# Optimization experiments

Measured on AMD Instinct MI355X. Metric: run time of the kernel, lower is better.

Reference implementation:

```python
import jax, jax.numpy as jnp
import numpy as np

A = 5.0  # smoothness parameter


def setup_inputs() -> dict:
    key = jax.random.key(0)
    kx, kw = jax.random.split(key)
    x = jax.random.uniform(kx, (4096, 256), dtype=jnp.float32)
    weight = jax.random.uniform(kw, (256, 256), dtype=jnp.float32)
    return {"x": x, "weight": weight}


def reference(x, weight):
    # inner: [batch, in_features, out_features] broadcast elementwise max
    inner = jnp.maximum(x[..., None], weight[None])
    # smooth min over in_features (dim=-2): -(1/a) * logsumexp(-a * inner)
    smooth = -jax.nn.logsumexp(-A * inner, axis=-2) / A
    # hard min over same dim
    hard = jnp.min(inner, axis=-2)
    # straight-through estimator: forward value = hard, gradient flows via smooth
    return jax.lax.stop_gradient(hard - smooth) + smooth
```

## Files before the change

kernel.cpp:

```cpp
#include <hip/hip_runtime.h>


typedef _Float16 h2 __attribute__((ext_vector_type(2)));
typedef int i16v __attribute__((ext_vector_type(16)));

__global__ __launch_bounds__(256)
void prepack_kernel(const float* __restrict__ x, const float* __restrict__ w,
                    unsigned int* __restrict__ xt, unsigned int* __restrict__ wq) {
    const int tid = blockIdx.x * 256 + threadIdx.x;
    if (tid < 524288) {
        const int j  = tid & 3;
        const int rr = (tid >> 2) & 3;
        const int c  = (tid >> 4) & 31;
        const int r4 = tid >> 9;
        const int row = (r4 << 2) + rr;
        const float2 v = *reinterpret_cast<const float2*>(&x[(size_t)row * 256 + (c << 3) + (j << 1)]);
        const h2 p = h2{(_Float16)v.x, (_Float16)v.y};
        xt[tid] = __builtin_bit_cast(unsigned int, p);
    } else {
        const int u   = tid - 524288;
        const int col = u & 255;
        const int j   = (u >> 8) & 3;
        const int c   = u >> 10;
        const int i0  = (c << 3) + (j << 1);
        const h2 p = h2{(_Float16)w[(size_t)i0 * 256 + col], (_Float16)w[(size_t)(i0 + 1) * 256 + col]};
        const int idx = ((((c >> 1) << 8) + col) << 3) + ((c & 1) << 2) + j;
        wq[(size_t)idx] = __builtin_bit_cast(unsigned int, p);
    }
}

#define PKSTEP(XS, WV, ACC) do { int _t;                                     \
    asm("v_pk_max_f16 %0, %2, %3\n\t"                                        \
        "v_pk_min_f16 %1, %1, %0"                                            \
        : "=&v"(_t), "+v"(ACC) : "s"(XS), "v"(WV)); } while (0)

#define STEPC(Xv, Wv) do {                                                   \
    PKSTEP(Xv[0],  Wv.x, acc0); PKSTEP(Xv[4],  Wv.x, acc1);                  \
    PKSTEP(Xv[8],  Wv.x, acc2); PKSTEP(Xv[12], Wv.x, acc3);                  \
    PKSTEP(Xv[1],  Wv.y, acc0); PKSTEP(Xv[5],  Wv.y, acc1);                  \
    PKSTEP(Xv[9],  Wv.y, acc2); PKSTEP(Xv[13], Wv.y, acc3);                  \
    PKSTEP(Xv[2],  Wv.z, acc0); PKSTEP(Xv[6],  Wv.z, acc1);                  \
    PKSTEP(Xv[10], Wv.z, acc2); PKSTEP(Xv[14], Wv.z, acc3);                  \
    PKSTEP(Xv[3],  Wv.w, acc0); PKSTEP(Xv[7],  Wv.w, acc1);                  \
    PKSTEP(Xv[11], Wv.w, acc2); PKSTEP(Xv[15], Wv.w, acc3); } while (0)

#define WAITALL() do {                                                       \
    asm volatile("s_waitcnt lgkmcnt(0) vmcnt(0)" ::: "memory");              \
    __builtin_amdgcn_sched_barrier(0); } while (0)

#define PF_SC(XA_, XB_, WA_, WB_, SC) do {                                   \
    const unsigned long long _xs = xa + (unsigned long long)(((SC) & 15) << 7); \
    const unsigned int _wo = wo + (unsigned int)(((SC) & 15) << 13);         \
    asm volatile("s_load_dwordx16 %0, %2, 0x0\n\t"                           \
                 "s_load_dwordx16 %1, %2, 0x40"                              \
                 : "=&s"(XA_), "=&s"(XB_) : "s"(_xs));                       \
    asm volatile("global_load_dwordx4 %0, %2, %3\n\t"                        \
                 "global_load_dwordx4 %1, %2, %3 offset:16"                  \
                 : "=&v"(WA_), "=&v"(WB_) : "v"(_wo), "s"(wb)); } while (0)

#define STAGE(K, CXA, CXB, CWA, CWB, NXA, NXB, NWA, NWB)                     \
    WAITALL();                                                               \
    if ((K) < 15) PF_SC(NXA, NXB, NWA, NWB, s0 + (K) + 1);                   \
    STEPC(CXA, CWA); STEPC(CXB, CWB);

__global__ __launch_bounds__(256, 4)
void stemm_main(const unsigned int* __restrict__ xt, const unsigned int* __restrict__ wq,
                float* __restrict__ out) {
    const int t    = threadIdx.x;
    const int lane = t & 63;
    const int wv   = __builtin_amdgcn_readfirstlane(t >> 6);
    const int c0   = (blockIdx.x & 3) << 6;
    const int rb   = blockIdx.x >> 2;
    const int r4   = (rb << 2) + wv;
    const int s0   = wv << 2;

    const unsigned long long xa = (unsigned long long)xt + ((unsigned long long)r4 << 11);
    const unsigned int       wo = (unsigned int)((c0 + lane) << 5);
    const unsigned long long wb = (unsigned long long)wq;

    i16v X0a{}, X0b{}, X1a{}, X1b{};
    uint4 W0a{0,0,0,0}, W0b{0,0,0,0}, W1a{0,0,0,0}, W1b{0,0,0,0};

    h2 acc0 = h2{(_Float16)65504.0f, (_Float16)65504.0f};
    h2 acc1 = acc0, acc2 = acc0, acc3 = acc0;

    PF_SC(X0a, X0b, W0a, W0b, s0);

    STAGE(0,  X0a, X0b, W0a, W0b,  X1a, X1b, W1a, W1b)
    STAGE(1,  X1a, X1b, W1a, W1b,  X0a, X0b, W0a, W0b)
    STAGE(2,  X0a, X0b, W0a, W0b,  X1a, X1b, W1a, W1b)
    STAGE(3,  X1a, X1b, W1a, W1b,  X0a, X0b, W0a, W0b)
    STAGE(4,  X0a, X0b, W0a, W0b,  X1a, X1b, W1a, W1b)
    STAGE(5,  X1a, X1b, W1a, W1b,  X0a, X0b, W0a, W0b)
    STAGE(6,  X0a, X0b, W0a, W0b,  X1a, X1b, W1a, W1b)
    STAGE(7,  X1a, X1b, W1a, W1b,  X0a, X0b, W0a, W0b)
    STAGE(8,  X0a, X0b, W0a, W0b,  X1a, X1b, W1a, W1b)
    STAGE(9,  X1a, X1b, W1a, W1b,  X0a, X0b, W0a, W0b)
    STAGE(10, X0a, X0b, W0a, W0b,  X1a, X1b, W1a, W1b)
    STAGE(11, X1a, X1b, W1a, W1b,  X0a, X0b, W0a, W0b)
    STAGE(12, X0a, X0b, W0a, W0b,  X1a, X1b, W1a, W1b)
    STAGE(13, X1a, X1b, W1a, W1b,  X0a, X0b, W0a, W0b)
    STAGE(14, X0a, X0b, W0a, W0b,  X1a, X1b, W1a, W1b)
    STAGE(15, X1a, X1b, W1a, W1b,  X0a, X0b, W0a, W0b)

    const int r0 = r4 << 2;
    out[(size_t)(r0 + 0) * 256 + c0 + lane] = fminf((float)acc0.x, (float)acc0.y);
    out[(size_t)(r0 + 1) * 256 + c0 + lane] = fminf((float)acc1.x, (float)acc1.y);
    out[(size_t)(r0 + 2) * 256 + c0 + lane] = fminf((float)acc2.x, (float)acc2.y);
    out[(size_t)(r0 + 3) * 256 + c0 + lane] = fminf((float)acc3.x, (float)acc3.y);
}

extern "C" void kernel_launch(void* const* d_in, const int* in_sizes, int n_in,
                              void* d_out, int out_size, void* d_ws, size_t ws_size,
                              hipStream_t stream) {
    const float* x = (const float*)d_in[0];
    const float* w = (const float*)d_in[1];
    float* out = (float*)d_out;

    unsigned int* xt = (unsigned int*)d_ws;
    unsigned int* wq = (unsigned int*)((char*)d_ws + (2u << 20));

    hipLaunchKernelGGL(prepack_kernel, dim3(2176), dim3(256), 0, stream, x, w, xt, wq);
    hipLaunchKernelGGL(stemm_main, dim3(1024), dim3(256), 0, stream, xt, wq, out);
}
```

Before: 21.40 us.

## Fuse fp16 prepack into main kernel, staging weights in LDS

```diff
diff --git a/kernel.cpp b/kernel.cpp
--- a/kernel.cpp
+++ b/kernel.cpp
@@ -4,29 +4,8 @@
 typedef _Float16 h2 __attribute__((ext_vector_type(2)));
 typedef int i16v __attribute__((ext_vector_type(16)));
 
-__global__ __launch_bounds__(256)
-void prepack_kernel(const float* __restrict__ x, const float* __restrict__ w,
-                    unsigned int* __restrict__ xt, unsigned int* __restrict__ wq) {
-    const int tid = blockIdx.x * 256 + threadIdx.x;
-    if (tid < 524288) {
-        const int j  = tid & 3;
-        const int rr = (tid >> 2) & 3;
-        const int c  = (tid >> 4) & 31;
-        const int r4 = tid >> 9;
-        const int row = (r4 << 2) + rr;
-        const float2 v = *reinterpret_cast<const float2*>(&x[(size_t)row * 256 + (c << 3) + (j << 1)]);
-        const h2 p = h2{(_Float16)v.x, (_Float16)v.y};
-        xt[tid] = __builtin_bit_cast(unsigned int, p);
-    } else {
-        const int u   = tid - 524288;
-        const int col = u & 255;
-        const int j   = (u >> 8) & 3;
-        const int c   = u >> 10;
-        const int i0  = (c << 3) + (j << 1);
-        const h2 p = h2{(_Float16)w[(size_t)i0 * 256 + col], (_Float16)w[(size_t)(i0 + 1) * 256 + col]};
-        const int idx = ((((c >> 1) << 8) + col) << 3) + ((c & 1) << 2) + j;
-        wq[(size_t)idx] = __builtin_bit_cast(unsigned int, p);
-    }
+static __device__ __forceinline__ unsigned int cvtpk(float a, float b) {
+    return __builtin_bit_cast(unsigned int, __builtin_amdgcn_cvt_pkrtz(a, b));
 }
 
 #define PKSTEP(XS, WV, ACC) do { int _t;                                     \
@@ -44,39 +23,74 @@
     PKSTEP(Xv[3],  Wv.w, acc0); PKSTEP(Xv[7],  Wv.w, acc1);                  \
     PKSTEP(Xv[11], Wv.w, acc2); PKSTEP(Xv[15], Wv.w, acc3); } while (0)
 
-#define WAITALL() do {                                                       \
-    asm volatile("s_waitcnt lgkmcnt(0) vmcnt(0)" ::: "memory");              \
+#define WAITL() do {                                                         \
+    asm volatile("s_waitcnt lgkmcnt(0)" ::: "memory");                       \
     __builtin_amdgcn_sched_barrier(0); } while (0)
 
 #define PF_SC(XA_, XB_, WA_, WB_, SC) do {                                   \
     const unsigned long long _xs = xa + (unsigned long long)(((SC) & 15) << 7); \
-    const unsigned int _wo = wo + (unsigned int)(((SC) & 15) << 13);         \
     asm volatile("s_load_dwordx16 %0, %2, 0x0\n\t"                           \
                  "s_load_dwordx16 %1, %2, 0x40"                              \
                  : "=&s"(XA_), "=&s"(XB_) : "s"(_xs));                       \
-    asm volatile("global_load_dwordx4 %0, %2, %3\n\t"                        \
-                 "global_load_dwordx4 %1, %2, %3 offset:16"                  \
-                 : "=&v"(WA_), "=&v"(WB_) : "v"(_wo), "s"(wb)); } while (0)
+    const unsigned int _wo = wob + (unsigned int)(((SC) & 15) << 11);        \
+    asm volatile("ds_read_b128 %0, %2\n\t"                                   \
+                 "ds_read_b128 %1, %2 offset:1024"                           \
+                 : "=&v"(WA_), "=&v"(WB_) : "v"(_wo)); } while (0)
 
 #define STAGE(K, CXA, CXB, CWA, CWB, NXA, NXB, NWA, NWB)                     \
-    WAITALL();                                                               \
+    WAITL();                                                                 \
     if ((K) < 15) PF_SC(NXA, NXB, NWA, NWB, s0 + (K) + 1);                   \
     STEPC(CXA, CWA); STEPC(CXB, CWB);
 
 __global__ __launch_bounds__(256, 4)
-void stemm_main(const unsigned int* __restrict__ xt, const unsigned int* __restrict__ wq,
-                float* __restrict__ out) {
+void stemm_fused(const float* __restrict__ x, const float* __restrict__ w,
+                 float* __restrict__ out, unsigned int* __restrict__ wsx) {
+    __shared__ __align__(16) unsigned char wlds[32768];
     const int t    = threadIdx.x;
     const int lane = t & 63;
     const int wv   = __builtin_amdgcn_readfirstlane(t >> 6);
     const int c0   = (blockIdx.x & 3) << 6;
     const int rb   = blockIdx.x >> 2;
-    const int r4   = (rb << 2) + wv;
-    const int s0   = wv << 2;
+    const int r0   = rb << 4;
+    unsigned int* xws = wsx + ((size_t)blockIdx.x << 11);
 
-    const unsigned long long xa = (unsigned long long)xt + ((unsigned long long)r4 << 11);
-    const unsigned int       wo = (unsigned int)((c0 + lane) << 5);
-    const unsigned long long wb = (unsigned long long)wq;
+    {
+        const int row = t >> 4, iq = t & 15;
+        const float4* xp = reinterpret_cast<const float4*>(&x[(size_t)(r0 + row) * 256 + (iq << 4)]);
+        const float4 a = xp[0], b = xp[1], c = xp[2], d = xp[3];
+        uint4 h0 = { cvtpk(a.x,a.y), cvtpk(a.z,a.w), cvtpk(b.x,b.y), cvtpk(b.z,b.w) };
+        uint4 h1 = { cvtpk(c.x,c.y), cvtpk(c.z,c.w), cvtpk(d.x,d.y), cvtpk(d.z,d.w) };
+        const int base = ((row >> 2) << 9) + (iq << 5) + ((row & 3) << 2);
+        *reinterpret_cast<uint4*>(xws + base)      = h0;
+        *reinterpret_cast<uint4*>(xws + base + 16) = h1;
+    }
+
+#pragma unroll
+    for (int uu = 0; uu < 4; ++uu) {
+        const int u    = (uu << 8) + t;
+        const int colp = u & 31;
+        const int k    = (u >> 5) & 1;
+        const int sc   = u >> 6;
+        const int i0   = (sc << 4) + (k << 3);
+        float2 v[8];
+#pragma unroll
+        for (int e = 0; e < 8; ++e)
+            v[e] = *reinterpret_cast<const float2*>(&w[(size_t)(i0 + e) * 256 + c0 + (colp << 1)]);
+        uint4 qa = { cvtpk(v[0].x,v[1].x), cvtpk(v[2].x,v[3].x), cvtpk(v[4].x,v[5].x), cvtpk(v[6].x,v[7].x) };
+        uint4 qb = { cvtpk(v[0].y,v[1].y), cvtpk(v[2].y,v[3].y), cvtpk(v[4].y,v[5].y), cvtpk(v[6].y,v[7].y) };
+        unsigned char* p = wlds + (sc << 11) + (k << 10) + (colp << 5);
+        *reinterpret_cast<uint4*>(p)      = qa;
+        *reinterpret_cast<uint4*>(p + 16) = qb;
+    }
+
+    asm volatile("s_waitcnt vmcnt(0) lgkmcnt(0)" ::: "memory");
+    __syncthreads();
+    asm volatile("s_dcache_inv\n\ts_nop 3" ::: "memory");
+    __builtin_amdgcn_sched_barrier(0);
+
+    const unsigned long long xa = (unsigned long long)xws + ((unsigned long long)wv << 11);
+    const unsigned int wob = (unsigned int)(unsigned long long)(wlds) + (unsigned int)(lane << 4);
+    const int s0 = wv << 2;
 
     i16v X0a{}, X0b{}, X1a{}, X1b{};
     uint4 W0a{0,0,0,0}, W0b{0,0,0,0}, W1a{0,0,0,0}, W1b{0,0,0,0};
@@ -103,11 +117,11 @@
     STAGE(14, X0a, X0b, W0a, W0b,  X1a, X1b, W1a, W1b)
     STAGE(15, X1a, X1b, W1a, W1b,  X0a, X0b, W0a, W0b)
 
-    const int r0 = r4 << 2;
-    out[(size_t)(r0 + 0) * 256 + c0 + lane] = fminf((float)acc0.x, (float)acc0.y);
-    out[(size_t)(r0 + 1) * 256 + c0 + lane] = fminf((float)acc1.x, (float)acc1.y);
-    out[(size_t)(r0 + 2) * 256 + c0 + lane] = fminf((float)acc2.x, (float)acc2.y);
-    out[(size_t)(r0 + 3) * 256 + c0 + lane] = fminf((float)acc3.x, (float)acc3.y);
+    const int orow = r0 + (wv << 2);
+    out[(size_t)(orow + 0) * 256 + c0 + lane] = fminf((float)acc0.x, (float)acc0.y);
+    out[(size_t)(orow + 1) * 256 + c0 + lane] = fminf((float)acc1.x, (float)acc1.y);
+    out[(size_t)(orow + 2) * 256 + c0 + lane] = fminf((float)acc2.x, (float)acc2.y);
+    out[(size_t)(orow + 3) * 256 + c0 + lane] = fminf((float)acc3.x, (float)acc3.y);
 }
 
 extern "C" void kernel_launch(void* const* d_in, const int* in_sizes, int n_in,
@@ -116,10 +130,7 @@
     const float* x = (const float*)d_in[0];
     const float* w = (const float*)d_in[1];
     float* out = (float*)d_out;
+    unsigned int* wsx = (unsigned int*)d_ws;
 
-    unsigned int* xt = (unsigned int*)d_ws;
-    unsigned int* wq = (unsigned int*)((char*)d_ws + (2u << 20));
-
-    hipLaunchKernelGGL(prepack_kernel, dim3(2176), dim3(256), 0, stream, x, w, xt, wq);
-    hipLaunchKernelGGL(stemm_main, dim3(1024), dim3(256), 0, stream, xt, wq, out);
+    hipLaunchKernelGGL(stemm_fused, dim3(1024), dim3(256), 0, stream, x, w, out, wsx);
 }
```

Measured after the change: 19.48 us. 1.1x faster.
